# Optimization experiments

Hardware: AMD Instinct MI355X
Metric: run time of the kernel (lower is better)

## Reference

```python
import jax, jax.numpy as jnp
import numpy as np

N = 100000          # nodes
E = 1_600_000       # edges (before self loops)
IN = 128            # in_channels
HID = 64            # hidden
HEADS = 4
EPS = 1e-5          # BatchNorm eps
NEG_SLOPE = 0.2     # GATConv leaky_relu slope


def setup_inputs() -> dict:
    key = jax.random.key(0)
    ks = jax.random.split(key, 16)
    he = lambda fan: (2.0 / fan) ** 0.5  # kaiming-normal scale
    d = {
        "x": jax.random.normal(ks[0], (N, IN), jnp.float32),
        "edge_index": jax.random.randint(ks[1], (2, E), 0, N, dtype=jnp.int64),
        "root_index": 0,
        "W1": jax.random.normal(ks[2], (IN, HEADS * HID), jnp.float32) * he(IN),
        "att_src1": jax.random.normal(ks[3], (HEADS, HID), jnp.float32) * 0.1,
        "att_dst1": jax.random.normal(ks[4], (HEADS, HID), jnp.float32) * 0.1,
        "b1": jnp.zeros((HEADS * HID,), jnp.float32),
        "W2": jax.random.normal(ks[5], (HEADS * HID, HID), jnp.float32) * he(HEADS * HID),
        "att_src2": jax.random.normal(ks[6], (1, HID), jnp.float32) * 0.1,
        "att_dst2": jax.random.normal(ks[7], (1, HID), jnp.float32) * 0.1,
        "b2": jnp.zeros((HID,), jnp.float32),
        "bn1_g": jnp.ones((HEADS * HID,), jnp.float32),
        "bn1_b": jnp.zeros((HEADS * HID,), jnp.float32),
        "bn1_m": jnp.zeros((HEADS * HID,), jnp.float32),
        "bn1_v": jnp.ones((HEADS * HID,), jnp.float32),
        "bn2_g": jnp.ones((HID,), jnp.float32),
        "bn2_b": jnp.zeros((HID,), jnp.float32),
        "bn2_m": jnp.zeros((HID,), jnp.float32),
        "bn2_v": jnp.ones((HID,), jnp.float32),
        "cg1_w": jax.random.normal(ks[8], (3 * HID, 64), jnp.float32) * he(3 * HID),
        "cg1_b": jnp.zeros((64,), jnp.float32),
        "cbn_g": jnp.ones((64,), jnp.float32),
        "cbn_b": jnp.zeros((64,), jnp.float32),
        "cbn_m": jnp.zeros((64,), jnp.float32),
        "cbn_v": jnp.ones((64,), jnp.float32),
        "cg2_w": jax.random.normal(ks[9], (64, 32), jnp.float32) * he(64),
        "cg2_b": jnp.zeros((32,), jnp.float32),
        "cg3_w": jax.random.normal(ks[10], (32, 1), jnp.float32) * he(32),
        "cg3_b": jnp.zeros((1,), jnp.float32),
    }
    return d


def _bn_eval(x, g, b, m, v):
    return (x - m) * jax.lax.rsqrt(v + EPS) * g + b


def _gat_conv(x, src, dst, W, att_src, att_dst, bias, heads, out_ch, concat):
    """PyG GATConv (eval mode, self loops already in src/dst)."""
    n = x.shape[0]
    h = (x @ W).reshape(n, heads, out_ch)                # [N,H,C]
    a_src = jnp.einsum('nhc,hc->nh', h, att_src)         # [N,H]
    a_dst = jnp.einsum('nhc,hc->nh', h, att_dst)
    e = jax.nn.leaky_relu(a_src[src] + a_dst[dst], NEG_SLOPE)   # [Etot,H]
    seg_max = jax.ops.segment_max(e, dst, num_segments=n)
    ex = jnp.exp(e - seg_max[dst])
    denom = jax.ops.segment_sum(ex, dst, num_segments=n)
    alpha = ex / (denom[dst] + 1e-16)                    # [Etot,H]
    msg = h[src] * alpha[:, :, None]                     # [Etot,H,C]
    out = jax.ops.segment_sum(msg, dst, num_segments=n)  # [N,H,C]
    if concat:
        return out.reshape(n, heads * out_ch) + bias
    return out.mean(axis=1) + bias


def reference(x, edge_index, root_index, W1, att_src1, att_dst1, b1,
              W2, att_src2, att_dst2, b2,
              bn1_g, bn1_b, bn1_m, bn1_v, bn2_g, bn2_b, bn2_m, bn2_v,
              cg1_w, cg1_b, cbn_g, cbn_b, cbn_m, cbn_v,
              cg2_w, cg2_b, cg3_w, cg3_b):
    n = x.shape[0]
    # add self loops (PyG GATConv default)
    loop = jnp.arange(n, dtype=edge_index.dtype)
    src = jnp.concatenate([edge_index[0], loop])
    dst = jnp.concatenate([edge_index[1], loop])

    h = _gat_conv(x, src, dst, W1, att_src1, att_dst1, b1, HEADS, HID, True)
    h = jax.nn.elu(_bn_eval(h, bn1_g, bn1_b, bn1_m, bn1_v))
    h = _gat_conv(h, src, dst, W2, att_src2, att_dst2, b2, 1, HID, False)
    node_emb = jax.nn.elu(_bn_eval(h, bn2_g, bn2_b, bn2_m, bn2_v))  # [N,HID]

    mean_emb = node_emb.mean(axis=0, keepdims=True)      # [1,HID]
    max_emb = node_emb.max(axis=0, keepdims=True)        # [1,HID]
    safe_root = min(root_index, n - 1)
    root_emb = node_emb[safe_root][None, :]              # single graph path
    g = jnp.concatenate([mean_emb, max_emb, root_emb], axis=-1)  # [1,3*HID]

    g = jax.nn.relu(_bn_eval(g @ cg1_w + cg1_b, cbn_g, cbn_b, cbn_m, cbn_v))
    g = jax.nn.relu(g @ cg2_w + cg2_b)
    logit = (g @ cg3_w + cg3_b).squeeze(-1)              # [1]
    return logit
```

## Files before the change

### kernel.cpp

```cpp
#include <hip/hip_runtime.h>

#define N_NODES 100000
#define N_EDGES 1600000
#define ETOT    1700000
#define IN_CH   128
#define C1      256
#define HID     64
#define BN_EPS  1e-5f
#define SLOPE   0.2f
#define NCHUNK  98
#define FILL_PH 8
#define PH_NODES 12500

typedef __attribute__((ext_vector_type(8))) short s16x8;
typedef __attribute__((ext_vector_type(4))) float f32x4;
#define MFMA16(a, b, c) __builtin_amdgcn_mfma_f32_16x16x32_bf16(a, b, c, 0, 0, 0)

__device__ __forceinline__ float leaky(float x) { return fmaxf(x, SLOPE * x); }
__device__ __forceinline__ float elu_f(float x) { return x > 0.f ? x : __expf(x) - 1.f; }
__device__ __forceinline__ unsigned short f2bf(float f) {
  unsigned int b = __float_as_uint(f);
  return (unsigned short)((b + 0x7FFFu + ((b >> 16) & 1u)) >> 16);
}
__device__ __forceinline__ float bf2f(unsigned short u) {
  return __uint_as_float((unsigned int)u << 16);
}

__global__ void __launch_bounds__(256) k_init_deg(int* __restrict__ deg) {
  int n = blockIdx.x * 256 + threadIdx.x;
  if (n < N_NODES) deg[n] = 1;
}

__global__ void __launch_bounds__(256) k_deg_ph(const int* __restrict__ edge, int* __restrict__ deg) {
  int bpp = (N_EDGES + 1023) >> 10;
  int ph = blockIdx.x / bpp;
  int lo = ph * PH_NODES, hi = lo + PH_NODES;
  int i0 = (blockIdx.x % bpp) * 1024 + threadIdx.x * 4;
  if (i0 >= N_EDGES) return;
  if (i0 + 3 < N_EDGES) {
    int4 dv = *(const int4*)(edge + N_EDGES + i0);
    if (dv.x >= lo && dv.x < hi) atomicAdd(&deg[dv.x], 1);
    if (dv.y >= lo && dv.y < hi) atomicAdd(&deg[dv.y], 1);
    if (dv.z >= lo && dv.z < hi) atomicAdd(&deg[dv.z], 1);
    if (dv.w >= lo && dv.w < hi) atomicAdd(&deg[dv.w], 1);
  } else {
    for (int j = 0; j < 4 && i0 + j < N_EDGES; j++) {
      int d = edge[N_EDGES + i0 + j];
      if (d >= lo && d < hi) atomicAdd(&deg[d], 1);
    }
  }
}

__global__ void __launch_bounds__(256) k_scan_part(const int* __restrict__ deg, int* __restrict__ part) {
  __shared__ int ls[256];
  int t = threadIdx.x;
  int base = blockIdx.x * 1024 + t * 4;
  int s = 0;
#pragma unroll
  for (int j = 0; j < 4; j++) if (base + j < N_NODES) s += deg[base + j];
  ls[t] = s;
  __syncthreads();
  for (int off = 128; off >= 1; off >>= 1) {
    if (t < off) ls[t] += ls[t + off];
    __syncthreads();
  }
  if (t == 0) part[blockIdx.x] = ls[0];
}

__global__ void k_scan_top(int* __restrict__ part, int* __restrict__ row_ptr) {
  if (threadIdx.x == 0 && blockIdx.x == 0) {
    int run = 0;
    for (int i = 0; i < NCHUNK; i++) { int t = part[i]; part[i] = run; run += t; }
    row_ptr[N_NODES] = run;
  }
}

__global__ void __launch_bounds__(256) k_scan_down(const int* __restrict__ deg, const int* __restrict__ part,
                                                   int* __restrict__ row_ptr, int* __restrict__ cursor) {
  __shared__ int ls[256];
  int t = threadIdx.x;
  int base = blockIdx.x * 1024 + t * 4;
  int v[4];
#pragma unroll
  for (int j = 0; j < 4; j++) v[j] = (base + j < N_NODES) ? deg[base + j] : 0;
  int tsum = v[0] + v[1] + v[2] + v[3];
  ls[t] = tsum;
  __syncthreads();
  for (int off = 1; off < 256; off <<= 1) {
    int add = (t >= off) ? ls[t - off] : 0;
    __syncthreads();
    ls[t] += add;
    __syncthreads();
  }
  int excl = ls[t] - tsum + part[blockIdx.x];
#pragma unroll
  for (int j = 0; j < 4; j++) {
    int idx = base + j;
    if (idx < N_NODES) { row_ptr[idx] = excl; cursor[idx] = excl; }
    excl += v[j];
  }
}

__global__ void __launch_bounds__(256) k_fill_ph(const int* __restrict__ edge, int* __restrict__ cursor,
                                                 const float* __restrict__ aS, const float* __restrict__ aD,
                                                 int* __restrict__ col, int* __restrict__ edst,
                                                 float* __restrict__ w1) {
  int bpp = (ETOT + 255) >> 8;
  int ph = blockIdx.x / bpp;
  int lo = ph * PH_NODES, hi = lo + PH_NODES;
  int i = (blockIdx.x % bpp) * 256 + threadIdx.x;
  if (i >= ETOT) return;
  int d = (i < N_EDGES) ? edge[N_EDGES + i] : (i - N_EDGES);
  if (d < lo || d >= hi) return;
  int s = (i < N_EDGES) ? edge[i] : d;
  int pos = atomicAdd(&cursor[d], 1);
  col[pos] = s;
  edst[pos] = d;
  float4 as4 = *(const float4*)(aS + (size_t)s * 4);
  float4 ad4 = *(const float4*)(aD + (size_t)d * 4);
  float4 w;
  w.x = __expf(fminf(leaky(as4.x + ad4.x), 80.f));
  w.y = __expf(fminf(leaky(as4.y + ad4.y), 80.f));
  w.z = __expf(fminf(leaky(as4.z + ad4.z), 80.f));
  w.w = __expf(fminf(leaky(as4.w + ad4.w), 80.f));
  *(float4*)(w1 + (size_t)pos * 4) = w;
}

__global__ void __launch_bounds__(256) k_w2(const int* __restrict__ col, const int* __restrict__ edst,
                                            const float* __restrict__ aS, const float* __restrict__ aD,
                                            float* __restrict__ w2) {
  int i = blockIdx.x * 256 + threadIdx.x;
  if (i >= ETOT) return;
  w2[i] = __expf(fminf(leaky(aS[col[i]] + aD[edst[i]]), 80.f));
}

__global__ void __launch_bounds__(256) k_prep(const float* __restrict__ W1, const float* __restrict__ W2,
                                              unsigned short* __restrict__ W1T, unsigned short* __restrict__ W2T) {
  int i = blockIdx.x * 256 + threadIdx.x;
  if (i < IN_CH * C1) {
    int k = i >> 8, c = i & 255;
    W1T[c * IN_CH + k] = f2bf(W1[i]);
  }
  if (i < C1 * HID) {
    int k = i >> 6, c = i & 63;
    W2T[c * C1 + k] = f2bf(W2[i]);
  }
}

__global__ void __launch_bounds__(256) k_gemm1(const float* __restrict__ x, const unsigned short* __restrict__ W1T,
                                               const float* __restrict__ attS, const float* __restrict__ attD,
                                               unsigned short* __restrict__ h1b, float* __restrict__ aS,
                                               float* __restrict__ aD) {
  __shared__ unsigned short As[64][IN_CH + 8];
  int tid = threadIdx.x;
  int w = tid >> 6, lane = tid & 63;
  int l15 = lane & 15, l4 = lane >> 4;
  int row0 = blockIdx.x * 64;
#pragma unroll
  for (int it = 0; it < 8; it++) {
    int idx = tid + it * 256;
    int r = idx >> 5;
    int k4 = (idx & 31) * 4;
    int gr = row0 + r; if (gr >= N_NODES) gr = N_NODES - 1;
    float4 v = *(const float4*)(x + (size_t)gr * IN_CH + k4);
    ushort4 bvec;
    bvec.x = f2bf(v.x); bvec.y = f2bf(v.y); bvec.z = f2bf(v.z); bvec.w = f2bf(v.w);
    *(ushort4*)&As[r][k4] = bvec;
  }
  __syncthreads();
  f32x4 acc[4][4];
#pragma unroll
  for (int mf = 0; mf < 4; mf++)
#pragma unroll
    for (int cf = 0; cf < 4; cf++) acc[mf][cf] = (f32x4){0.f, 0.f, 0.f, 0.f};
#pragma unroll
  for (int ks = 0; ks < 4; ks++) {
    int koff = ks * 32 + l4 * 8;
    s16x8 a[4];
#pragma unroll
    for (int mf = 0; mf < 4; mf++) a[mf] = *(const s16x8*)&As[mf * 16 + l15][koff];
#pragma unroll
    for (int cf = 0; cf < 4; cf++) {
      s16x8 b = *(const s16x8*)(W1T + (size_t)(w * 64 + cf * 16 + l15) * IN_CH + koff);
#pragma unroll
      for (int mf = 0; mf < 4; mf++) acc[mf][cf] = MFMA16(a[mf], b, acc[mf][cf]);
    }
  }
  float as_c[4], ad_c[4];
#pragma unroll
  for (int cf = 0; cf < 4; cf++) {
    as_c[cf] = attS[w * HID + cf * 16 + l15];
    ad_c[cf] = attD[w * HID + cf * 16 + l15];
  }
#pragma unroll
  for (int mf = 0; mf < 4; mf++) {
#pragma unroll
    for (int reg = 0; reg < 4; reg++) {
      int gr = row0 + mf * 16 + l4 * 4 + reg;
      bool ok = gr < N_NODES;
      float s = 0.f, dd = 0.f;
#pragma unroll
      for (int cf = 0; cf < 4; cf++) {
        float v = acc[mf][cf][reg];
        if (ok) h1b[(size_t)gr * C1 + w * 64 + cf * 16 + l15] = f2bf(v);
        s += v * as_c[cf];
        dd += v * ad_c[cf];
      }
#pragma unroll
      for (int m = 1; m <= 8; m <<= 1) { s += __shfl_xor(s, m, 64); dd += __shfl_xor(dd, m, 64); }
      if (ok && l15 == 0) {
        aS[(size_t)gr * 4 + w] = s;
        aD[(size_t)gr * 4 + w] = dd;
      }
    }
  }
}

__global__ void __launch_bounds__(256) k_agg1(const int* __restrict__ row_ptr, const int* __restrict__ col,
                                              const float* __restrict__ w1,
                                              const unsigned short* __restrict__ h1b, const float* __restrict__ b1,
                                              const float* __restrict__ g1, const float* __restrict__ be1,
                                              const float* __restrict__ m1, const float* __restrict__ v1,
                                              unsigned short* __restrict__ hmb) {
  int wave = threadIdx.x >> 6;
  int lane = threadIdx.x & 63;
  int d = blockIdx.x * 4 + wave;
  if (d >= N_NODES) return;
  int head = lane >> 4;
  int s0 = row_ptr[d], s1 = row_ptr[d + 1];
  float denom = 0.f;
  float4 acc = {0.f, 0.f, 0.f, 0.f};
  int c0 = lane * 4;
  int i = s0;
  int iend8 = s0 + ((s1 - s0) & ~7);
  for (; i < iend8; i += 8) {
    int cv = col[i + (lane & 7)];
    int sid[8];
#pragma unroll
    for (int j = 0; j < 8; j++) sid[j] = __builtin_amdgcn_readfirstlane(__shfl(cv, j));
    float wv[8];
#pragma unroll
    for (int j = 0; j < 8; j++) wv[j] = w1[(size_t)(i + j) * 4 + head];
    ushort4 h[8];
#pragma unroll
    for (int j = 0; j < 8; j++) h[j] = *(const ushort4*)(h1b + ((size_t)sid[j] << 8) + c0);
#pragma unroll
    for (int j = 0; j < 8; j++) {
      denom += wv[j];
      acc.x += wv[j] * bf2f(h[j].x);
      acc.y += wv[j] * bf2f(h[j].y);
      acc.z += wv[j] * bf2f(h[j].z);
      acc.w += wv[j] * bf2f(h[j].w);
    }
  }
  for (; i < s1; i++) {
    int s = __builtin_amdgcn_readfirstlane(col[i]);
    float wv = w1[(size_t)i * 4 + head];
    ushort4 hv = *(const ushort4*)(h1b + ((size_t)s << 8) + c0);
    denom += wv;
    acc.x += wv * bf2f(hv.x);
    acc.y += wv * bf2f(hv.y);
    acc.z += wv * bf2f(hv.z);
    acc.w += wv * bf2f(hv.w);
  }
  float inv = 1.f / (denom + 1e-16f);
  float4 bb = *(const float4*)(b1 + c0);
  float4 gg = *(const float4*)(g1 + c0);
  float4 be = *(const float4*)(be1 + c0);
  float4 mm = *(const float4*)(m1 + c0);
  float4 vv = *(const float4*)(v1 + c0);
  ushort4 o;
  o.x = f2bf(elu_f((acc.x * inv + bb.x - mm.x) * rsqrtf(vv.x + BN_EPS) * gg.x + be.x));
  o.y = f2bf(elu_f((acc.y * inv + bb.y - mm.y) * rsqrtf(vv.y + BN_EPS) * gg.y + be.y));
  o.z = f2bf(elu_f((acc.z * inv + bb.z - mm.z) * rsqrtf(vv.z + BN_EPS) * gg.z + be.z));
  o.w = f2bf(elu_f((acc.w * inv + bb.w - mm.w) * rsqrtf(vv.w + BN_EPS) * gg.w + be.w));
  *(ushort4*)(hmb + (size_t)d * C1 + c0) = o;
}

__global__ void __launch_bounds__(256) k_gemm2(const unsigned short* __restrict__ hmb, const unsigned short* __restrict__ W2T,
                                               const float* __restrict__ attS, const float* __restrict__ attD,
                                               unsigned short* __restrict__ h2b, float* __restrict__ aS,
                                               float* __restrict__ aD) {
  __shared__ unsigned short As[64][C1 + 8];
  int tid = threadIdx.x;
  int w = tid >> 6, lane = tid & 63;
  int l15 = lane & 15, l4 = lane >> 4;
  int row0 = blockIdx.x * 64;
#pragma unroll
  for (int it = 0; it < 8; it++) {
    int idx = tid + it * 256;
    int r = idx >> 5;
    int k8 = (idx & 31) * 8;
    int gr = row0 + r; if (gr >= N_NODES) gr = N_NODES - 1;
    *(uint4*)&As[r][k8] = *(const uint4*)(hmb + (size_t)gr * C1 + k8);
  }
  __syncthreads();
  f32x4 acc[4];
#pragma unroll
  for (int cf = 0; cf < 4; cf++) acc[cf] = (f32x4){0.f, 0.f, 0.f, 0.f};
#pragma unroll
  for (int ks = 0; ks < 8; ks++) {
    int koff = ks * 32 + l4 * 8;
    s16x8 a = *(const s16x8*)&As[w * 16 + l15][koff];
#pragma unroll
    for (int cf = 0; cf < 4; cf++) {
      s16x8 b = *(const s16x8*)(W2T + (size_t)(cf * 16 + l15) * C1 + koff);
      acc[cf] = MFMA16(a, b, acc[cf]);
    }
  }
  float as_c[4], ad_c[4];
#pragma unroll
  for (int cf = 0; cf < 4; cf++) {
    as_c[cf] = attS[cf * 16 + l15];
    ad_c[cf] = attD[cf * 16 + l15];
  }
#pragma unroll
  for (int reg = 0; reg < 4; reg++) {
    int gr = row0 + w * 16 + l4 * 4 + reg;
    bool ok = gr < N_NODES;
    float s = 0.f, dd = 0.f;
#pragma unroll
    for (int cf = 0; cf < 4; cf++) {
      float v = acc[cf][reg];
      if (ok) h2b[(size_t)gr * HID + cf * 16 + l15] = f2bf(v);
      s += v * as_c[cf];
      dd += v * ad_c[cf];
    }
#pragma unroll
    for (int m = 1; m <= 8; m <<= 1) { s += __shfl_xor(s, m, 64); dd += __shfl_xor(dd, m, 64); }
    if (ok && l15 == 0) { aS[gr] = s; aD[gr] = dd; }
  }
}

__global__ void __launch_bounds__(256) k_agg2(const int* __restrict__ row_ptr, const int* __restrict__ col,
                                              const float* __restrict__ w2,
                                              const unsigned short* __restrict__ h2b, const float* __restrict__ b2,
                                              const float* __restrict__ g2, const float* __restrict__ be2,
                                              const float* __restrict__ m2, const float* __restrict__ v2,
                                              float* __restrict__ emb) {
  int wave = threadIdx.x >> 6;
  int lane = threadIdx.x & 63;
  int d = blockIdx.x * 4 + wave;
  if (d >= N_NODES) return;
  int s0 = row_ptr[d], s1 = row_ptr[d + 1];
  float denom = 0.f, acc = 0.f;
  int i = s0;
  int iend8 = s0 + ((s1 - s0) & ~7);
  for (; i < iend8; i += 8) {
    int cv = col[i + (lane & 7)];
    int sid[8];
#pragma unroll
    for (int j = 0; j < 8; j++) sid[j] = __builtin_amdgcn_readfirstlane(__shfl(cv, j));
    float wv[8];
#pragma unroll
    for (int j = 0; j < 8; j++) wv[j] = w2[i + j];
    unsigned short h[8];
#pragma unroll
    for (int j = 0; j < 8; j++) h[j] = h2b[((size_t)sid[j] << 6) + lane];
#pragma unroll
    for (int j = 0; j < 8; j++) {
      denom += wv[j];
      acc += wv[j] * bf2f(h[j]);
    }
  }
  for (; i < s1; i++) {
    int s = __builtin_amdgcn_readfirstlane(col[i]);
    float wv = w2[i];
    unsigned short hv = h2b[((size_t)s << 6) + lane];
    denom += wv;
    acc += wv * bf2f(hv);
  }
  float o = acc / (denom + 1e-16f) + b2[lane];
  o = (o - m2[lane]) * rsqrtf(v2[lane] + BN_EPS) * g2[lane] + be2[lane];
  emb[(size_t)d * HID + lane] = elu_f(o);
}

__global__ void __launch_bounds__(256) k_pool(const float* __restrict__ emb, float* __restrict__ psum,
                                              float* __restrict__ pmax) {
  __shared__ float ss[4][64], sm[4][64];
  int t = threadIdx.x;
  int c = t & 63, rg = t >> 6;
  float s = 0.f, m = -INFINITY;
  for (int n = blockIdx.x * 4 + rg; n < N_NODES; n += gridDim.x * 4) {
    float v = emb[(size_t)n * HID + c];
    s += v; m = fmaxf(m, v);
  }
  ss[rg][c] = s; sm[rg][c] = m;
  __syncthreads();
  if (t < 64) {
    psum[blockIdx.x * 64 + t] = ss[0][t] + ss[1][t] + ss[2][t] + ss[3][t];
    pmax[blockIdx.x * 64 + t] = fmaxf(fmaxf(sm[0][t], sm[1][t]), fmaxf(sm[2][t], sm[3][t]));
  }
}

__global__ void __launch_bounds__(256) k_final(const float* __restrict__ psum, const float* __restrict__ pmax,
                                               const float* __restrict__ emb, const int* __restrict__ rootp,
                                               const float* __restrict__ cg1w, const float* __restrict__ cg1b,
                                               const float* __restrict__ cbng, const float* __restrict__ cbnb,
                                               const float* __restrict__ cbnm, const float* __restrict__ cbnv,
                                               const float* __restrict__ cg2w, const float* __restrict__ cg2b,
                                               const float* __restrict__ cg3w, const float* __restrict__ cg3b,
                                               float* __restrict__ out) {
  __shared__ float ss[4][64], sm[4][64];
  __shared__ float g[192], t1[64], t2[32];
  int t = threadIdx.x;
  int c = t & 63, q = t >> 6;
  float s = 0.f, m = -INFINITY;
  for (int b = q; b < 256; b += 4) {
    s += psum[b * 64 + c];
    m = fmaxf(m, pmax[b * 64 + c]);
  }
  ss[q][c] = s; sm[q][c] = m;
  __syncthreads();
  if (t < 64) {
    float tot = ss[0][t] + ss[1][t] + ss[2][t] + ss[3][t];
    float mx = fmaxf(fmaxf(sm[0][t], sm[1][t]), fmaxf(sm[2][t], sm[3][t]));
    int root = rootp[0];
    if (root > N_NODES - 1) root = N_NODES - 1;
    if (root < 0) root = 0;
    g[t] = tot / (float)N_NODES;
    g[64 + t] = mx;
    g[128 + t] = emb[(size_t)root * HID + t];
  }
  __syncthreads();
  if (t < 64) {
    float o = cg1b[t];
    for (int i = 0; i < 192; i++) o += g[i] * cg1w[i * 64 + t];
    o = (o - cbnm[t]) * rsqrtf(cbnv[t] + BN_EPS) * cbng[t] + cbnb[t];
    t1[t] = o > 0.f ? o : 0.f;
  }
  __syncthreads();
  if (t < 32) {
    float o = cg2b[t];
    for (int i = 0; i < 64; i++) o += t1[i] * cg2w[i * 32 + t];
    t2[t] = o > 0.f ? o : 0.f;
  }
  __syncthreads();
  if (t == 0) {
    float o = cg3b[0];
    for (int i = 0; i < 32; i++) o += t2[i] * cg3w[i];
    out[0] = o;
  }
}

extern "C" void kernel_launch(void* const* d_in, const int* in_sizes, int n_in,
                              void* d_out, int out_size, void* d_ws, size_t ws_size,
                              hipStream_t stream) {
  const float* x     = (const float*)d_in[0];
  const int*   edge  = (const int*)d_in[1];
  const int*   root  = (const int*)d_in[2];
  const float* W1    = (const float*)d_in[3];
  const float* attS1 = (const float*)d_in[4];
  const float* attD1 = (const float*)d_in[5];
  const float* b1    = (const float*)d_in[6];
  const float* W2    = (const float*)d_in[7];
  const float* attS2 = (const float*)d_in[8];
  const float* attD2 = (const float*)d_in[9];
  const float* b2    = (const float*)d_in[10];
  const float* bn1g  = (const float*)d_in[11];
  const float* bn1b  = (const float*)d_in[12];
  const float* bn1m  = (const float*)d_in[13];
  const float* bn1v  = (const float*)d_in[14];
  const float* bn2g  = (const float*)d_in[15];
  const float* bn2b  = (const float*)d_in[16];
  const float* bn2m  = (const float*)d_in[17];
  const float* bn2v  = (const float*)d_in[18];
  const float* cg1w  = (const float*)d_in[19];
  const float* cg1b  = (const float*)d_in[20];
  const float* cbng  = (const float*)d_in[21];
  const float* cbnb  = (const float*)d_in[22];
  const float* cbnm  = (const float*)d_in[23];
  const float* cbnv  = (const float*)d_in[24];
  const float* cg2w  = (const float*)d_in[25];
  const float* cg2b  = (const float*)d_in[26];
  const float* cg3w  = (const float*)d_in[27];
  const float* cg3b  = (const float*)d_in[28];

  char* ws = (char*)d_ws;
  size_t off = 0;
  auto carve = [&](size_t bytes) { char* p = ws + off; off += (bytes + 255) & ~(size_t)255; return p; };
  unsigned short* h1b = (unsigned short*)carve((size_t)N_NODES * C1 * 2);
  unsigned short* hmb = (unsigned short*)carve((size_t)N_NODES * C1 * 2);
  float* aS1     = (float*)carve((size_t)N_NODES * 4 * 4);
  float* aD1     = (float*)carve((size_t)N_NODES * 4 * 4);
  int*   deg     = (int*)  carve((size_t)N_NODES * 4);
  int*   row_ptr = (int*)  carve((size_t)(N_NODES + 1) * 4);
  int*   cursor  = (int*)  carve((size_t)N_NODES * 4);
  int*   col     = (int*)  carve((size_t)ETOT * 4);
  int*   edst    = (int*)  carve((size_t)ETOT * 4);
  float* w1      = (float*)carve((size_t)ETOT * 4 * 4);
  int*   part    = (int*)  carve(512);
  unsigned short* W1T = (unsigned short*)carve((size_t)IN_CH * C1 * 2);
  unsigned short* W2T = (unsigned short*)carve((size_t)C1 * HID * 2);
  unsigned short* h2b = h1b;
  float* aS2  = (float*)(h1b + (size_t)N_NODES * HID);
  float* aD2  = aS2 + N_NODES;
  float* w2   = w1;
  float* emb  = (float*)hmb;
  float* psum = emb + (size_t)N_NODES * HID;
  float* pmax = psum + 256 * 64;

  int bpp_deg  = (N_EDGES + 1023) >> 10;
  int bpp_fill = (ETOT + 255) >> 8;
  k_init_deg<<<(N_NODES + 255) / 256, 256, 0, stream>>>(deg);
  k_deg_ph<<<bpp_deg * FILL_PH, 256, 0, stream>>>(edge, deg);
  k_prep<<<(IN_CH * C1 + 255) / 256, 256, 0, stream>>>(W1, W2, W1T, W2T);
  k_gemm1<<<(N_NODES + 63) / 64, 256, 0, stream>>>(x, W1T, attS1, attD1, h1b, aS1, aD1);
  k_scan_part<<<NCHUNK, 256, 0, stream>>>(deg, part);
  k_scan_top<<<1, 64, 0, stream>>>(part, row_ptr);
  k_scan_down<<<NCHUNK, 256, 0, stream>>>(deg, part, row_ptr, cursor);
  k_fill_ph<<<bpp_fill * FILL_PH, 256, 0, stream>>>(edge, cursor, aS1, aD1, col, edst, w1);
  k_agg1<<<(N_NODES + 3) / 4, 256, 0, stream>>>(row_ptr, col, w1, h1b, b1, bn1g, bn1b, bn1m, bn1v, hmb);
  k_gemm2<<<(N_NODES + 63) / 64, 256, 0, stream>>>(hmb, W2T, attS2, attD2, h2b, aS2, aD2);
  k_w2<<<(ETOT + 255) / 256, 256, 0, stream>>>(col, edst, aS2, aD2, w2);
  k_agg2<<<(N_NODES + 3) / 4, 256, 0, stream>>>(row_ptr, col, w2, h2b, b2, bn2g, bn2b, bn2m, bn2v, emb);
  k_pool<<<256, 256, 0, stream>>>(emb, psum, pmax);
  k_final<<<1, 256, 0, stream>>>(psum, pmax, emb, root, cg1w, cg1b, cbng, cbnb, cbnm, cbnv,
                                 cg2w, cg2b, cg3w, cg3b, (float*)d_out);
}
```

Before: 517.8 us.

## Fuse layer-2 edge weight computation into aggregation and drop edst array

Removes the separate k_w2 kernel and the per-edge destination array. Layer-2 attention weights are now computed inside k_agg2 from gathered aS values and the node's aD, which avoids writing and re-reading a per-edge weight buffer. Both aggregation kernels replace the scalar tail loop with a masked 8-wide final iteration using clamped indices. The fill kernel is also split into 12 destination-range phases instead of 8. The cost is extra exp work and an extra gather of aS per edge inside agg2, plus more passes over the edge list in fill.

```diff
diff --git a/kernel.cpp b/kernel.cpp
--- a/kernel.cpp
+++ b/kernel.cpp
@@ -9,8 +9,10 @@
 #define BN_EPS  1e-5f
 #define SLOPE   0.2f
 #define NCHUNK  98
-#define FILL_PH 8
-#define PH_NODES 12500
+#define DEG_PH  8
+#define DEG_PHN 12500
+#define FILL_PH 12
+#define FILL_PHN 8334
 
 typedef __attribute__((ext_vector_type(8))) short s16x8;
 typedef __attribute__((ext_vector_type(4))) float f32x4;
@@ -34,7 +36,7 @@
 __global__ void __launch_bounds__(256) k_deg_ph(const int* __restrict__ edge, int* __restrict__ deg) {
   int bpp = (N_EDGES + 1023) >> 10;
   int ph = blockIdx.x / bpp;
-  int lo = ph * PH_NODES, hi = lo + PH_NODES;
+  int lo = ph * DEG_PHN, hi = lo + DEG_PHN;
   int i0 = (blockIdx.x % bpp) * 1024 + threadIdx.x * 4;
   if (i0 >= N_EDGES) return;
   if (i0 + 3 < N_EDGES) {
@@ -103,11 +105,10 @@
 
 __global__ void __launch_bounds__(256) k_fill_ph(const int* __restrict__ edge, int* __restrict__ cursor,
                                                  const float* __restrict__ aS, const float* __restrict__ aD,
-                                                 int* __restrict__ col, int* __restrict__ edst,
-                                                 float* __restrict__ w1) {
+                                                 int* __restrict__ col, float* __restrict__ w1) {
   int bpp = (ETOT + 255) >> 8;
   int ph = blockIdx.x / bpp;
-  int lo = ph * PH_NODES, hi = lo + PH_NODES;
+  int lo = ph * FILL_PHN, hi = lo + FILL_PHN;
   int i = (blockIdx.x % bpp) * 256 + threadIdx.x;
   if (i >= ETOT) return;
   int d = (i < N_EDGES) ? edge[N_EDGES + i] : (i - N_EDGES);
@@ -115,7 +116,6 @@
   int s = (i < N_EDGES) ? edge[i] : d;
   int pos = atomicAdd(&cursor[d], 1);
   col[pos] = s;
-  edst[pos] = d;
   float4 as4 = *(const float4*)(aS + (size_t)s * 4);
   float4 ad4 = *(const float4*)(aD + (size_t)d * 4);
   float4 w;
@@ -124,14 +124,6 @@
   w.z = __expf(fminf(leaky(as4.z + ad4.z), 80.f));
   w.w = __expf(fminf(leaky(as4.w + ad4.w), 80.f));
   *(float4*)(w1 + (size_t)pos * 4) = w;
-}
-
-__global__ void __launch_bounds__(256) k_w2(const int* __restrict__ col, const int* __restrict__ edst,
-                                            const float* __restrict__ aS, const float* __restrict__ aD,
-                                            float* __restrict__ w2) {
-  int i = blockIdx.x * 256 + threadIdx.x;
-  if (i >= ETOT) return;
-  w2[i] = __expf(fminf(leaky(aS[col[i]] + aD[edst[i]]), 80.f));
 }
 
 __global__ void __launch_bounds__(256) k_prep(const float* __restrict__ W1, const float* __restrict__ W2,
@@ -228,19 +220,24 @@
   if (d >= N_NODES) return;
   int head = lane >> 4;
   int s0 = row_ptr[d], s1 = row_ptr[d + 1];
+  int s1m1 = s1 - 1;
   float denom = 0.f;
   float4 acc = {0.f, 0.f, 0.f, 0.f};
   int c0 = lane * 4;
-  int i = s0;
-  int iend8 = s0 + ((s1 - s0) & ~7);
-  for (; i < iend8; i += 8) {
-    int cv = col[i + (lane & 7)];
+  for (int base = s0; base < s1; base += 8) {
+    int left = s1 - base;
+    int idx = base + (lane & 7); if (idx > s1m1) idx = s1m1;
+    int cv = col[idx];
     int sid[8];
 #pragma unroll
     for (int j = 0; j < 8; j++) sid[j] = __builtin_amdgcn_readfirstlane(__shfl(cv, j));
     float wv[8];
 #pragma unroll
-    for (int j = 0; j < 8; j++) wv[j] = w1[(size_t)(i + j) * 4 + head];
+    for (int j = 0; j < 8; j++) {
+      int wi = base + j; if (wi > s1m1) wi = s1m1;
+      float wl = w1[(size_t)wi * 4 + head];
+      wv[j] = (j < left) ? wl : 0.f;
+    }
     ushort4 h[8];
 #pragma unroll
     for (int j = 0; j < 8; j++) h[j] = *(const ushort4*)(h1b + ((size_t)sid[j] << 8) + c0);
@@ -252,16 +249,6 @@
       acc.z += wv[j] * bf2f(h[j].z);
       acc.w += wv[j] * bf2f(h[j].w);
     }
-  }
-  for (; i < s1; i++) {
-    int s = __builtin_amdgcn_readfirstlane(col[i]);
-    float wv = w1[(size_t)i * 4 + head];
-    ushort4 hv = *(const ushort4*)(h1b + ((size_t)s << 8) + c0);
-    denom += wv;
-    acc.x += wv * bf2f(hv.x);
-    acc.y += wv * bf2f(hv.y);
-    acc.z += wv * bf2f(hv.z);
-    acc.w += wv * bf2f(hv.w);
   }
   float inv = 1.f / (denom + 1e-16f);
   float4 bb = *(const float4*)(b1 + c0);
@@ -333,7 +320,7 @@
 }
 
 __global__ void __launch_bounds__(256) k_agg2(const int* __restrict__ row_ptr, const int* __restrict__ col,
-                                              const float* __restrict__ w2,
+                                              const float* __restrict__ aS, const float* __restrict__ aD,
                                               const unsigned short* __restrict__ h2b, const float* __restrict__ b2,
                                               const float* __restrict__ g2, const float* __restrict__ be2,
                                               const float* __restrict__ m2, const float* __restrict__ v2,
@@ -342,33 +329,34 @@
   int lane = threadIdx.x & 63;
   int d = blockIdx.x * 4 + wave;
   if (d >= N_NODES) return;
+  float ad = aD[d];
   int s0 = row_ptr[d], s1 = row_ptr[d + 1];
+  int s1m1 = s1 - 1;
   float denom = 0.f, acc = 0.f;
-  int i = s0;
-  int iend8 = s0 + ((s1 - s0) & ~7);
-  for (; i < iend8; i += 8) {
-    int cv = col[i + (lane & 7)];
+  for (int base = s0; base < s1; base += 8) {
+    int left = s1 - base;
+    int idx = base + (lane & 7); if (idx > s1m1) idx = s1m1;
+    int cv = col[idx];
     int sid[8];
 #pragma unroll
     for (int j = 0; j < 8; j++) sid[j] = __builtin_amdgcn_readfirstlane(__shfl(cv, j));
+    float e[8];
+#pragma unroll
+    for (int j = 0; j < 8; j++) e[j] = aS[sid[j]];
+    unsigned short h[8];
+#pragma unroll
+    for (int j = 0; j < 8; j++) h[j] = h2b[((size_t)sid[j] << 6) + lane];
     float wv[8];
 #pragma unroll
-    for (int j = 0; j < 8; j++) wv[j] = w2[i + j];
-    unsigned short h[8];
-#pragma unroll
-    for (int j = 0; j < 8; j++) h[j] = h2b[((size_t)sid[j] << 6) + lane];
+    for (int j = 0; j < 8; j++) {
+      float wl = __expf(fminf(leaky(e[j] + ad), 80.f));
+      wv[j] = (j < left) ? wl : 0.f;
+    }
 #pragma unroll
     for (int j = 0; j < 8; j++) {
       denom += wv[j];
       acc += wv[j] * bf2f(h[j]);
     }
-  }
-  for (; i < s1; i++) {
-    int s = __builtin_amdgcn_readfirstlane(col[i]);
-    float wv = w2[i];
-    unsigned short hv = h2b[((size_t)s << 6) + lane];
-    denom += wv;
-    acc += wv * bf2f(hv);
   }
   float o = acc / (denom + 1e-16f) + b2[lane];
   o = (o - m2[lane]) * rsqrtf(v2[lane] + BN_EPS) * g2[lane] + be2[lane];
@@ -487,7 +475,6 @@
   int*   row_ptr = (int*)  carve((size_t)(N_NODES + 1) * 4);
   int*   cursor  = (int*)  carve((size_t)N_NODES * 4);
   int*   col     = (int*)  carve((size_t)ETOT * 4);
-  int*   edst    = (int*)  carve((size_t)ETOT * 4);
   float* w1      = (float*)carve((size_t)ETOT * 4 * 4);
   int*   part    = (int*)  carve(512);
   unsigned short* W1T = (unsigned short*)carve((size_t)IN_CH * C1 * 2);
@@ -495,7 +482,6 @@
   unsigned short* h2b = h1b;
   float* aS2  = (float*)(h1b + (size_t)N_NODES * HID);
   float* aD2  = aS2 + N_NODES;
-  float* w2   = w1;
   float* emb  = (float*)hmb;
   float* psum = emb + (size_t)N_NODES * HID;
   float* pmax = psum + 256 * 64;
@@ -503,17 +489,16 @@
   int bpp_deg  = (N_EDGES + 1023) >> 10;
   int bpp_fill = (ETOT + 255) >> 8;
   k_init_deg<<<(N_NODES + 255) / 256, 256, 0, stream>>>(deg);
-  k_deg_ph<<<bpp_deg * FILL_PH, 256, 0, stream>>>(edge, deg);
+  k_deg_ph<<<bpp_deg * DEG_PH, 256, 0, stream>>>(edge, deg);
   k_prep<<<(IN_CH * C1 + 255) / 256, 256, 0, stream>>>(W1, W2, W1T, W2T);
   k_gemm1<<<(N_NODES + 63) / 64, 256, 0, stream>>>(x, W1T, attS1, attD1, h1b, aS1, aD1);
   k_scan_part<<<NCHUNK, 256, 0, stream>>>(deg, part);
   k_scan_top<<<1, 64, 0, stream>>>(part, row_ptr);
   k_scan_down<<<NCHUNK, 256, 0, stream>>>(deg, part, row_ptr, cursor);
-  k_fill_ph<<<bpp_fill * FILL_PH, 256, 0, stream>>>(edge, cursor, aS1, aD1, col, edst, w1);
+  k_fill_ph<<<bpp_fill * FILL_PH, 256, 0, stream>>>(edge, cursor, aS1, aD1, col, w1);
   k_agg1<<<(N_NODES + 3) / 4, 256, 0, stream>>>(row_ptr, col, w1, h1b, b1, bn1g, bn1b, bn1m, bn1v, hmb);
   k_gemm2<<<(N_NODES + 63) / 64, 256, 0, stream>>>(hmb, W2T, attS2, attD2, h2b, aS2, aD2);
-  k_w2<<<(ETOT + 255) / 256, 256, 0, stream>>>(col, edst, aS2, aD2, w2);
-  k_agg2<<<(N_NODES + 3) / 4, 256, 0, stream>>>(row_ptr, col, w2, h2b, b2, bn2g, bn2b, bn2m, bn2v, emb);
+  k_agg2<<<(N_NODES + 3) / 4, 256, 0, stream>>>(row_ptr, col, aS2, aD2, h2b, b2, bn2g, bn2b, bn2m, bn2v, emb);
   k_pool<<<256, 256, 0, stream>>>(emb, psum, pmax);
   k_final<<<1, 256, 0, stream>>>(psum, pmax, emb, root, cg1w, cg1b, cbng, cbnb, cbnm, cbnv,
                                  cg2w, cg2b, cg3w, cg3b, (float*)d_out);
```

Result: no change. 507.9 us (-1.9%).
